# Performance work log

Measured on AMD Instinct MI355X. Metric: run time of the kernel, lower is better.

The kernel has to match this reference:

```python
import jax, jax.numpy as jnp
import numpy as np

EMBED_DIM = 512
NUM_HEADS = 8
TGT_LEN = 1024
BSZ = 16


def setup_inputs() -> dict:
    key = jax.random.key(0)
    ks = jax.random.split(key, 6)
    E = EMBED_DIM
    query = jax.random.normal(ks[0], (TGT_LEN, BSZ, E), jnp.float32)
    i_proj = jax.random.normal(ks[1], (3 * E,), jnp.float32)
    # xavier_uniform-ish scale for (3E, E)
    lim = (6.0 / (3 * E + E)) ** 0.5
    in_proj_weight = jax.random.uniform(ks[2], (3 * E, E), jnp.float32, -lim, lim)
    in_proj_bias = jnp.zeros((3 * E,), jnp.float32)
    lim2 = (6.0 / (2 * E)) ** 0.5
    out_w = jax.random.uniform(ks[3], (E, E), jnp.float32, -lim2, lim2)
    out_b = jnp.zeros((E,), jnp.float32)
    bias_k = jax.random.normal(ks[4], (1, 1, E), jnp.float32)
    bias_v = jax.random.normal(ks[5], (1, 1, E), jnp.float32)
    return dict(query=query, i_proj=i_proj, in_proj_weight=in_proj_weight,
                in_proj_bias=in_proj_bias, out_w=out_w, out_b=out_b,
                bias_k=bias_k, bias_v=bias_v)


def reference(query, i_proj, in_proj_weight, in_proj_bias, out_w, out_b, bias_k, bias_v):
    # qkv_same path: key = value = query (self-attention)
    T, B, E = query.shape
    H = NUM_HEADS
    hd = E // H
    scaling = hd ** -0.5
    # per-call weight mutation: every 3rd column replaced by i_proj
    w = in_proj_weight.at[:, ::3].set(i_proj[:, None])
    qkv = jnp.einsum('tbe,fe->tbf', query, w) + in_proj_bias  # (T, B, 3E)
    q, k, v = jnp.split(qkv, 3, axis=-1)
    q = q * scaling
    k = jnp.concatenate([k, jnp.broadcast_to(bias_k, (1, B, E))], axis=0)  # (T+1, B, E)
    v = jnp.concatenate([v, jnp.broadcast_to(bias_v, (1, B, E))], axis=0)
    S = k.shape[0]
    q = q.reshape(T, B * H, hd).transpose(1, 0, 2)  # (B*H, T, hd)
    k = k.reshape(S, B * H, hd).transpose(1, 0, 2)  # (B*H, S, hd)
    v = v.reshape(S, B * H, hd).transpose(1, 0, 2)
    aw = jnp.einsum('nth,nsh->nts', q, k)  # (B*H, T, S)
    # global min-max normalization over the entire score tensor (not softmax)
    mn = jnp.min(aw)
    mx = jnp.max(aw)
    aw = (aw - mn) / (mx - mn)
    attn = jnp.einsum('nts,nsh->nth', aw, v)  # (B*H, T, hd)
    attn = attn.transpose(1, 0, 2).reshape(T, B, E)
    attn = attn @ out_w.T + out_b  # out_proj
    aw_avg = aw.reshape(B, H, T, S).sum(axis=1) / H  # (B, T, S)
    wq, wk, wv = jnp.split(w, 3, axis=0)
    w_ret = jnp.stack([wq.T, wk.T, wv.T], axis=0)  # (3, E, E)
    return attn, aw_avg, w_ret
```

## Files before the change

kernel.cpp:

```cpp
#include <hip/hip_runtime.h>
#include <hip/hip_bf16.h>
#include <stdint.h>

typedef __bf16 bf16;
typedef __bf16 bf16x8 __attribute__((ext_vector_type(8)));
typedef __bf16 bf16x4 __attribute__((ext_vector_type(4)));
typedef float  f32x4  __attribute__((ext_vector_type(4)));

#define MFMA_BF16(a,b,c) __builtin_amdgcn_mfma_f32_16x16x32_bf16((a),(b),(c),0,0,0)

#define WS_QBF_IN  0L
#define WS_WBF     16777216L
#define WS_OUTWBF  18350080L
#define WS_Q       18874368L
#define WS_K       35651584L
#define WS_V       52428800L
#define WS_VT      69206016L
#define WS_AWLAST  85983232L
#define WS_VCS     86507520L
#define WS_MM      86540288L
#define WS_KT      86540544L
#define WS_KTV     103317760L

__device__ __forceinline__ void gload16(const void* g, void* l) {
  __builtin_amdgcn_global_load_lds((const __attribute__((address_space(1))) uint32_t*)g,
                                   (__attribute__((address_space(3))) uint32_t*)l, 16, 0, 0);
}
__device__ __forceinline__ unsigned ordf(float x) {
  unsigned b = __float_as_uint(x);
  return (b & 0x80000000u) ? ~b : (b | 0x80000000u);
}
__device__ __forceinline__ float deordf(unsigned u) {
  unsigned b = (u & 0x80000000u) ? (u ^ 0x80000000u) : ~u;
  return __uint_as_float(b);
}

__global__ __launch_bounds__(256) void cvt_query_kernel(const float* __restrict__ in,
                                                        bf16* __restrict__ out) {
  long i = (long)blockIdx.x * 256 + threadIdx.x;
  for (; i < 2097152L; i += (long)gridDim.x * 256) {
    float4 v = ((const float4*)in)[i];
    bf16x4 o; o[0] = (bf16)v.x; o[1] = (bf16)v.y; o[2] = (bf16)v.z; o[3] = (bf16)v.w;
    ((bf16x4*)out)[i] = o;
  }
}

__global__ __launch_bounds__(256) void prep_weights_kernel(
    const float* __restrict__ in_w, const float* __restrict__ i_proj,
    const float* __restrict__ out_w, bf16* __restrict__ w_bf,
    bf16* __restrict__ outw_bf, float* __restrict__ w_ret,
    unsigned* __restrict__ mm) {
  long idx = (long)blockIdx.x * 256 + threadIdx.x;
  if (idx == 0) { mm[0] = 0xFFFFFFFFu; mm[1] = 0u; }
  if (idx < 786432L) {
    int f = (int)(idx >> 9), e = (int)(idx & 511);
    float val = (e % 3 == 0) ? i_proj[f] : in_w[idx];
    w_bf[idx] = (bf16)val;
    w_ret[(long)(f >> 9) * 262144 + (long)e * 512 + (f & 511)] = val;
  } else if (idx < 1048576L) {
    long j = idx - 786432L;
    outw_bf[j] = (bf16)out_w[j];
  }
}

template <int MODE>
__global__ __launch_bounds__(256, 2) void gemm_kernel(
    const bf16* __restrict__ A, const bf16* __restrict__ B,
    const float* __restrict__ bias,
    bf16* __restrict__ q_out, bf16* __restrict__ k_out, bf16* __restrict__ v_out,
    float* __restrict__ outC) {
  const int K = 512;
  __shared__ __align__(16) bf16 aTile[128 * 32];
  __shared__ __align__(16) bf16 bTile[128 * 32];
  const int tid = threadIdx.x;
  const int lane = tid & 63, w = tid >> 6;
  const int l15 = lane & 15, l4 = lane >> 4;
  const long r0 = (long)blockIdx.y * 128;
  const long f0 = (long)blockIdx.x * 128;
  const int rm = (w >> 1) * 64, cn = (w & 1) * 64;
  const int srow = tid >> 2;
  const int scc = tid & 3;
  f32x4 acc[4][4] = {};

  for (int kk = 0; kk < K; kk += 32) {
#pragma unroll
    for (int i = 0; i < 2; ++i) {
      int row = srow + i * 64;
      int cc = scc ^ (row & 3);
      gload16(A + (r0 + row) * K + kk + cc * 8, (char*)aTile + (w * 64 + i * 256) * 16);
    }
#pragma unroll
    for (int i = 0; i < 2; ++i) {
      int row = srow + i * 64;
      int cc = scc ^ (row & 3);
      gload16(B + (f0 + row) * K + kk + cc * 8, (char*)bTile + (w * 64 + i * 256) * 16);
    }
    __syncthreads();
    bf16x8 af[4], bfr[4];
#pragma unroll
    for (int mi = 0; mi < 4; ++mi) {
      int r = rm + mi * 16 + l15;
      int c = l4 ^ (r & 3);
      af[mi] = *(const bf16x8*)((const char*)aTile + r * 64 + c * 16);
    }
#pragma unroll
    for (int ni = 0; ni < 4; ++ni) {
      int r = cn + ni * 16 + l15;
      int c = l4 ^ (r & 3);
      bfr[ni] = *(const bf16x8*)((const char*)bTile + r * 64 + c * 16);
    }
#pragma unroll
    for (int mi = 0; mi < 4; ++mi)
#pragma unroll
      for (int ni = 0; ni < 4; ++ni)
        acc[mi][ni] = MFMA_BF16(af[mi], bfr[ni], acc[mi][ni]);
    __syncthreads();
  }
#pragma unroll
  for (int mi = 0; mi < 4; ++mi)
#pragma unroll
    for (int ni = 0; ni < 4; ++ni)
#pragma unroll
      for (int r = 0; r < 4; ++r) {
        long row = r0 + rm + mi * 16 + l4 * 4 + r;
        int f = (int)f0 + cn + ni * 16 + l15;
        float val = acc[mi][ni][r] + bias[f];
        if (MODE == 0) {
          int t = (int)(row >> 4), b = (int)(row & 15);
          int which = f >> 9, hh = (f >> 6) & 7, d = f & 63;
          long off = ((long)(b * 8 + hh) * 1024 + t) * 64 + d;
          if (which == 0)      q_out[off] = (bf16)(val * 0.125f);
          else if (which == 1) k_out[off] = (bf16)val;
          else                 v_out[off] = (bf16)val;
        } else {
          outC[row * 512 + f] = val;
        }
      }
}

__global__ __launch_bounds__(256, 2) void awsum_gemm_kernel(
    const bf16* __restrict__ q_bf, const bf16* __restrict__ k_bf,
    const unsigned* __restrict__ mm, float* __restrict__ aw_out) {
  __shared__ __align__(16) bf16 aTile[128 * 32];
  __shared__ __align__(16) bf16 bTile[128 * 32];
  const int tid = threadIdx.x;
  const int lane = tid & 63, w = tid >> 6;
  const int l15 = lane & 15, l4 = lane >> 4;
  const int b = blockIdx.z;
  const int t0 = blockIdx.y * 128;
  const int s0 = blockIdx.x * 128;
  const int rm = (w >> 1) * 64, cn = (w & 1) * 64;
  const int srow = tid >> 2;
  const int scc = tid & 3;
  f32x4 acc[4][4] = {};

  for (int kk = 0; kk < 512; kk += 32) {
    int h = kk >> 6, db = kk & 63;
#pragma unroll
    for (int i = 0; i < 2; ++i) {
      int row = srow + i * 64;
      int cc = scc ^ (row & 3);
      gload16(q_bf + ((long)(b * 8 + h) * 1024 + t0 + row) * 64 + db + cc * 8,
              (char*)aTile + (w * 64 + i * 256) * 16);
    }
#pragma unroll
    for (int i = 0; i < 2; ++i) {
      int row = srow + i * 64;
      int cc = scc ^ (row & 3);
      gload16(k_bf + ((long)(b * 8 + h) * 1024 + s0 + row) * 64 + db + cc * 8,
              (char*)bTile + (w * 64 + i * 256) * 16);
    }
    __syncthreads();
    bf16x8 af[4], bfr[4];
#pragma unroll
    for (int mi = 0; mi < 4; ++mi) {
      int r = rm + mi * 16 + l15;
      int c = l4 ^ (r & 3);
      af[mi] = *(const bf16x8*)((const char*)aTile + r * 64 + c * 16);
    }
#pragma unroll
    for (int ni = 0; ni < 4; ++ni) {
      int r = cn + ni * 16 + l15;
      int c = l4 ^ (r & 3);
      bfr[ni] = *(const bf16x8*)((const char*)bTile + r * 64 + c * 16);
    }
#pragma unroll
    for (int mi = 0; mi < 4; ++mi)
#pragma unroll
      for (int ni = 0; ni < 4; ++ni)
        acc[mi][ni] = MFMA_BF16(af[mi], bfr[ni], acc[mi][ni]);
    __syncthreads();
  }
  float mn = deordf(mm[0]), mx = deordf(mm[1]);
  float a8 = 0.125f / (mx - mn), c = -mn * 8.f * a8;
#pragma unroll
  for (int mi = 0; mi < 4; ++mi)
#pragma unroll
    for (int ni = 0; ni < 4; ++ni)
#pragma unroll
      for (int r = 0; r < 4; ++r) {
        int t = t0 + rm + mi * 16 + l4 * 4 + r;
        int s = s0 + cn + ni * 16 + l15;
        aw_out[((long)b * 1024 + t) * 1025 + s] = fmaf(a8, acc[mi][ni][r], c);
      }
}

__global__ __launch_bounds__(256) void transpose_kv_kernel(
    const bf16* __restrict__ k_bf, const bf16* __restrict__ v_bf,
    bf16* __restrict__ kT, bf16* __restrict__ vT) {
  const bf16* src = blockIdx.z ? v_bf : k_bf;
  bf16* dst = blockIdx.z ? vT : kT;
  const int n = blockIdx.y;
  const long s0 = (long)blockIdx.x * 64;
  __shared__ __align__(16) bf16 tile[64][72];
  const int tid = threadIdx.x;
  const int row = tid >> 3, cc = tid & 7;
#pragma unroll
  for (int it = 0; it < 2; ++it) {
    int r = row + it * 32;
    bf16x8 vv = *(const bf16x8*)(src + ((long)n * 1024 + s0 + r) * 64 + cc * 8);
    *(bf16x8*)&tile[r][cc * 8] = vv;
  }
  __syncthreads();
#pragma unroll
  for (int it = 0; it < 2; ++it) {
    int d = row + it * 32;
    bf16x8 ov;
#pragma unroll
    for (int j = 0; j < 8; ++j) ov[j] = tile[cc * 8 + j][d];
    *(bf16x8*)(dst + ((long)n * 64 + d) * 1024 + s0 + cc * 8) = ov;
  }
}

__global__ __launch_bounds__(256) void vcolsum_kernel(const bf16* __restrict__ v_bf,
                                                      const float* __restrict__ bias_v,
                                                      float* __restrict__ vcs) {
  const int n = blockIdx.x, h = n & 7;
  const int d = threadIdx.x & 63, g = threadIdx.x >> 6;
  float acc = 0.f;
  const bf16* base = v_bf + (long)n * 65536 + d;
  for (int s = g * 256; s < g * 256 + 256; ++s) acc += (float)base[(long)s * 64];
  __shared__ float red[4][64];
  red[g][d] = acc;
  __syncthreads();
  if (g == 0) vcs[n * 64 + d] = red[0][d] + red[1][d] + red[2][d] + red[3][d] + bias_v[h * 64 + d];
}

__global__ __launch_bounds__(256, 2) void qkt_minmax_kernel(
    const bf16* __restrict__ q_bf, const bf16* __restrict__ k_bf,
    unsigned* __restrict__ mm) {
  const int tid = threadIdx.x;
  const int lane = tid & 63, w = tid >> 6;
  const int l15 = lane & 15, l4 = lane >> 4;
  const int d_ = blockIdx.x;
  const int xcd = d_ & 7, slot = d_ >> 3;
  const int b = xcd * 2 + (slot >> 6);
  const int rest = slot & 63;
  const int t0 = (rest >> 2) * 64;
  const int h = ((rest >> 1) & 1) * 4 + w;
  const int sh = rest & 1;
  const long n = (long)b * 8 + h;

  bf16x8 qf[4][2];
  const bf16* qbase = q_bf + (n * 1024 + t0) * 64;
#pragma unroll
  for (int mi = 0; mi < 4; ++mi)
#pragma unroll
    for (int ks = 0; ks < 2; ++ks)
      qf[mi][ks] = *(const bf16x8*)(qbase + (mi * 16 + l15) * 64 + ks * 32 + l4 * 8);

  const bf16* kbase = k_bf + n * 65536 + (long)sh * 32768;

  float vmin = 1e30f, vmax = -1e30f;
  for (int st = 0; st < 16; ++st) {
    const int s0 = st * 32;
    bf16x8 kf[4];
#pragma unroll
    for (int ks = 0; ks < 2; ++ks)
#pragma unroll
      for (int ni = 0; ni < 2; ++ni)
        kf[ks * 2 + ni] =
            *(const bf16x8*)(kbase + (long)(s0 + ni * 16 + l15) * 64 + ks * 32 + l4 * 8);
    f32x4 aw[4][2] = {};
#pragma unroll
    for (int ks = 0; ks < 2; ++ks)
#pragma unroll
      for (int mi = 0; mi < 4; ++mi)
#pragma unroll
        for (int ni = 0; ni < 2; ++ni)
          aw[mi][ni] = MFMA_BF16(qf[mi][ks], kf[ks * 2 + ni], aw[mi][ni]);
#pragma unroll
    for (int mi = 0; mi < 4; ++mi)
#pragma unroll
      for (int ni = 0; ni < 2; ++ni)
#pragma unroll
        for (int r = 0; r < 4; ++r) {
          vmin = fminf(vmin, aw[mi][ni][r]);
          vmax = fmaxf(vmax, aw[mi][ni][r]);
        }
  }
#pragma unroll
  for (int off = 32; off; off >>= 1) {
    vmin = fminf(vmin, __shfl_xor(vmin, off));
    vmax = fmaxf(vmax, __shfl_xor(vmax, off));
  }
  if (lane == 0) { atomicMin(&mm[0], ordf(vmin)); atomicMax(&mm[1], ordf(vmax)); }
}

__global__ __launch_bounds__(256) void ktv_kernel(const bf16* __restrict__ kT,
                                                  const bf16* __restrict__ vT,
                                                  bf16* __restrict__ ktvT) {
  const int n = blockIdx.x;
  const int tid = threadIdx.x;
  const int lane = tid & 63, w = tid >> 6;
  const int l15 = lane & 15, l4 = lane >> 4;
  const int wr = w >> 1, wc = w & 1;
  f32x4 acc[2][2] = {};
  const bf16* kbase = kT + (long)n * 65536;
  const bf16* vbase = vT + (long)n * 65536;
  for (int s0 = 0; s0 < 1024; s0 += 32) {
    bf16x8 af[2], bfr[2];
#pragma unroll
    for (int mi = 0; mi < 2; ++mi)
      af[mi] = *(const bf16x8*)(kbase + (long)(wr * 32 + mi * 16 + l15) * 1024 + s0 + l4 * 8);
#pragma unroll
    for (int ni = 0; ni < 2; ++ni)
      bfr[ni] = *(const bf16x8*)(vbase + (long)(wc * 32 + ni * 16 + l15) * 1024 + s0 + l4 * 8);
#pragma unroll
    for (int mi = 0; mi < 2; ++mi)
#pragma unroll
      for (int ni = 0; ni < 2; ++ni)
        acc[mi][ni] = MFMA_BF16(af[mi], bfr[ni], acc[mi][ni]);
  }
#pragma unroll
  for (int mi = 0; mi < 2; ++mi)
#pragma unroll
    for (int ni = 0; ni < 2; ++ni)
#pragma unroll
      for (int r = 0; r < 4; ++r) {
        int d = wr * 32 + mi * 16 + l4 * 4 + r;
        int dp = wc * 32 + ni * 16 + l15;
        ktvT[(long)n * 4096 + dp * 64 + d] = (bf16)acc[mi][ni][r];
      }
}

__global__ __launch_bounds__(256) void qattn_kernel(
    const bf16* __restrict__ q_bf, const bf16* __restrict__ ktvT,
    const float* __restrict__ aw_last, const float* __restrict__ vcs,
    const float* __restrict__ bias_v, const unsigned* __restrict__ mm,
    bf16* __restrict__ A2) {
  const int tid = threadIdx.x;
  const int lane = tid & 63, w = tid >> 6;
  const int l15 = lane & 15, l4 = lane >> 4;
  const int t0 = blockIdx.x * 64;
  const int h = blockIdx.y * 4 + w;
  const int b = blockIdx.z;
  const long n = (long)b * 8 + h;
  f32x4 acc[4][4] = {};
  const bf16* qbase = q_bf + (n * 1024 + t0) * 64;
  const bf16* kbase = ktvT + (long)n * 4096;
#pragma unroll
  for (int kk = 0; kk < 64; kk += 32) {
    bf16x8 af[4], bfr[4];
#pragma unroll
    for (int mi = 0; mi < 4; ++mi)
      af[mi] = *(const bf16x8*)(qbase + (mi * 16 + l15) * 64 + kk + l4 * 8);
#pragma unroll
    for (int ni = 0; ni < 4; ++ni)
      bfr[ni] = *(const bf16x8*)(kbase + (ni * 16 + l15) * 64 + kk + l4 * 8);
#pragma unroll
    for (int mi = 0; mi < 4; ++mi)
#pragma unroll
      for (int ni = 0; ni < 4; ++ni)
        acc[mi][ni] = MFMA_BF16(af[mi], bfr[ni], acc[mi][ni]);
  }
  float mn = deordf(mm[0]), mx = deordf(mm[1]);
  float a = 1.f / (mx - mn), c = -mn * a;
#pragma unroll
  for (int mi = 0; mi < 4; ++mi)
#pragma unroll
    for (int r = 0; r < 4; ++r) {
      int t = t0 + mi * 16 + l4 * 4 + r;
      float alast = a * aw_last[n * 1024 + t];
#pragma unroll
      for (int ni = 0; ni < 4; ++ni) {
        int dp = ni * 16 + l15;
        float val = a * acc[mi][ni][r] + alast * bias_v[h * 64 + dp] + c * vcs[n * 64 + dp];
        A2[((long)t * 16 + b) * 512 + h * 64 + dp] = (bf16)val;
      }
    }
}

__global__ __launch_bounds__(256) void bias_col_kernel(const bf16* __restrict__ q_bf,
                                                       const float* __restrict__ bias_k,
                                                       float* __restrict__ aw_last,
                                                       unsigned* __restrict__ mm) {
  const int n = blockIdx.y, h = n & 7;
  const int t = blockIdx.x * 256 + threadIdx.x;
  float acc = 0.f;
  const bf16* qrow = q_bf + ((long)n * 1024 + t) * 64;
#pragma unroll
  for (int j = 0; j < 8; ++j) {
    bf16x8 qv = *(const bf16x8*)(qrow + j * 8);
#pragma unroll
    for (int e = 0; e < 8; ++e) acc += (float)qv[e] * bias_k[h * 64 + j * 8 + e];
  }
  aw_last[(long)n * 1024 + t] = acc;
  float vmin = acc, vmax = acc;
#pragma unroll
  for (int off = 32; off; off >>= 1) {
    vmin = fminf(vmin, __shfl_xor(vmin, off));
    vmax = fmaxf(vmax, __shfl_xor(vmax, off));
  }
  if ((threadIdx.x & 63) == 0) { atomicMin(&mm[0], ordf(vmin)); atomicMax(&mm[1], ordf(vmax)); }
}

__global__ __launch_bounds__(256) void lastcol_kernel(const float* __restrict__ aw_last,
                                                      const unsigned* __restrict__ mm,
                                                      float* __restrict__ aw_out) {
  int idx = blockIdx.x * 256 + threadIdx.x;
  int b = idx >> 10, t = idx & 1023;
  float mn = deordf(mm[0]), mx = deordf(mm[1]);
  float a8 = 0.125f / (mx - mn), c = -mn * 8.f * a8;
  float sum = 0.f;
#pragma unroll
  for (int h = 0; h < 8; ++h) sum += aw_last[(long)(b * 8 + h) * 1024 + t];
  aw_out[((long)b * 1024 + t) * 1025 + 1024] = fmaf(a8, sum, c);
}

extern "C" void kernel_launch(void* const* d_in, const int* in_sizes, int n_in,
                              void* d_out, int out_size, void* d_ws, size_t ws_size,
                              hipStream_t stream) {
  const float* query  = (const float*)d_in[0];
  const float* i_proj = (const float*)d_in[1];
  const float* in_w   = (const float*)d_in[2];
  const float* in_b   = (const float*)d_in[3];
  const float* out_w  = (const float*)d_in[4];
  const float* out_b  = (const float*)d_in[5];
  const float* bias_k = (const float*)d_in[6];
  const float* bias_v = (const float*)d_in[7];
  float* out = (float*)d_out;

  char* ws = (char*)d_ws;
  bf16* qbf_in = (bf16*)(ws + WS_QBF_IN);
  bf16* w_bf   = (bf16*)(ws + WS_WBF);
  bf16* outwbf = (bf16*)(ws + WS_OUTWBF);
  bf16* q_bf   = (bf16*)(ws + WS_Q);
  bf16* k_bf   = (bf16*)(ws + WS_K);
  bf16* v_bf   = (bf16*)(ws + WS_V);
  bf16* vT     = (bf16*)(ws + WS_VT);
  bf16* kT     = (bf16*)(ws + WS_KT);
  bf16* ktvT   = (bf16*)(ws + WS_KTV);
  float* aw_last = (float*)(ws + WS_AWLAST);
  float* vcs     = (float*)(ws + WS_VCS);
  unsigned* mm   = (unsigned*)(ws + WS_MM);
  bf16* A2 = qbf_in;

  float* out_attn  = out;
  float* out_awavg = out + 8388608L;
  float* out_wret  = out + 25182208L;

  cvt_query_kernel<<<2048, 256, 0, stream>>>(query, qbf_in);
  prep_weights_kernel<<<4096, 256, 0, stream>>>(in_w, i_proj, out_w, w_bf, outwbf, out_wret, mm);
  gemm_kernel<0><<<dim3(12, 128), 256, 0, stream>>>(qbf_in, w_bf, in_b, q_bf, k_bf, v_bf, nullptr);
  transpose_kv_kernel<<<dim3(16, 128, 2), 256, 0, stream>>>(k_bf, v_bf, kT, vT);
  vcolsum_kernel<<<128, 256, 0, stream>>>(v_bf, bias_v, vcs);
  qkt_minmax_kernel<<<1024, 256, 0, stream>>>(q_bf, k_bf, mm);
  bias_col_kernel<<<dim3(4, 128), 256, 0, stream>>>(q_bf, bias_k, aw_last, mm);
  ktv_kernel<<<128, 256, 0, stream>>>(kT, vT, ktvT);
  awsum_gemm_kernel<<<dim3(8, 8, 16), 256, 0, stream>>>(q_bf, k_bf, mm, out_awavg);
  lastcol_kernel<<<64, 256, 0, stream>>>(aw_last, mm, out_awavg);
  qattn_kernel<<<dim3(16, 2, 16), 256, 0, stream>>>(q_bf, ktvT, aw_last, vcs, bias_v, mm, A2);
  gemm_kernel<1><<<dim3(4, 128), 256, 0, stream>>>(A2, outwbf, out_b, nullptr, nullptr, nullptr, out_attn);
}
```

Measured before the change: 337.0 us.

## Fuse global min-max into head-summed score GEMM and rescale in separate pass

Removes the standalone QK^T min/max kernel. The head-summed score GEMM now accumulates each head separately, folding per-head min/max into atomics and writing raw head sums. A new elementwise pass then normalises the whole (B,T,S+1) output, including the bias column. This avoids recomputing all QK^T products a second time, at the cost of an extra full read and write of the 67 MB averaged-weights output and more register pressure for the per-head accumulators.

Result: faster. 322.5 us (-4.3%).

```diff
diff --git a/kernel.cpp b/kernel.cpp
--- a/kernel.cpp
+++ b/kernel.cpp
@@ -140,7 +140,7 @@
 
 __global__ __launch_bounds__(256, 2) void awsum_gemm_kernel(
     const bf16* __restrict__ q_bf, const bf16* __restrict__ k_bf,
-    const unsigned* __restrict__ mm, float* __restrict__ aw_out) {
+    float* __restrict__ aw_raw, unsigned* __restrict__ mm) {
   __shared__ __align__(16) bf16 aTile[128 * 32];
   __shared__ __align__(16) bf16 bTile[128 * 32];
   const int tid = threadIdx.x;
@@ -153,6 +153,8 @@
   const int srow = tid >> 2;
   const int scc = tid & 3;
   f32x4 acc[4][4] = {};
+  f32x4 hsum[4][4] = {};
+  float vmin = 1e30f, vmax = -1e30f;
 
   for (int kk = 0; kk < 512; kk += 32) {
     int h = kk >> 6, db = kk & 63;
@@ -190,9 +192,21 @@
       for (int ni = 0; ni < 4; ++ni)
         acc[mi][ni] = MFMA_BF16(af[mi], bfr[ni], acc[mi][ni]);
     __syncthreads();
-  }
-  float mn = deordf(mm[0]), mx = deordf(mm[1]);
-  float a8 = 0.125f / (mx - mn), c = -mn * 8.f * a8;
+    if (kk & 32) {
+#pragma unroll
+      for (int mi = 0; mi < 4; ++mi)
+#pragma unroll
+        for (int ni = 0; ni < 4; ++ni) {
+#pragma unroll
+          for (int r = 0; r < 4; ++r) {
+            float v = acc[mi][ni][r];
+            vmin = fminf(vmin, v); vmax = fmaxf(vmax, v);
+            hsum[mi][ni][r] += v;
+          }
+          acc[mi][ni] = (f32x4){0.f, 0.f, 0.f, 0.f};
+        }
+    }
+  }
 #pragma unroll
   for (int mi = 0; mi < 4; ++mi)
 #pragma unroll
@@ -201,8 +215,14 @@
       for (int r = 0; r < 4; ++r) {
         int t = t0 + rm + mi * 16 + l4 * 4 + r;
         int s = s0 + cn + ni * 16 + l15;
-        aw_out[((long)b * 1024 + t) * 1025 + s] = fmaf(a8, acc[mi][ni][r], c);
+        aw_raw[((long)b * 1024 + t) * 1025 + s] = hsum[mi][ni][r];
       }
+#pragma unroll
+  for (int off = 32; off; off >>= 1) {
+    vmin = fminf(vmin, __shfl_xor(vmin, off));
+    vmax = fmaxf(vmax, __shfl_xor(vmax, off));
+  }
+  if (lane == 0) { atomicMin(&mm[0], ordf(vmin)); atomicMax(&mm[1], ordf(vmax)); }
 }
 
 __global__ __launch_bounds__(256) void transpose_kv_kernel(
@@ -244,67 +264,6 @@
   red[g][d] = acc;
   __syncthreads();
   if (g == 0) vcs[n * 64 + d] = red[0][d] + red[1][d] + red[2][d] + red[3][d] + bias_v[h * 64 + d];
-}
-
-__global__ __launch_bounds__(256, 2) void qkt_minmax_kernel(
-    const bf16* __restrict__ q_bf, const bf16* __restrict__ k_bf,
-    unsigned* __restrict__ mm) {
-  const int tid = threadIdx.x;
-  const int lane = tid & 63, w = tid >> 6;
-  const int l15 = lane & 15, l4 = lane >> 4;
-  const int d_ = blockIdx.x;
-  const int xcd = d_ & 7, slot = d_ >> 3;
-  const int b = xcd * 2 + (slot >> 6);
-  const int rest = slot & 63;
-  const int t0 = (rest >> 2) * 64;
-  const int h = ((rest >> 1) & 1) * 4 + w;
-  const int sh = rest & 1;
-  const long n = (long)b * 8 + h;
-
-  bf16x8 qf[4][2];
-  const bf16* qbase = q_bf + (n * 1024 + t0) * 64;
-#pragma unroll
-  for (int mi = 0; mi < 4; ++mi)
-#pragma unroll
-    for (int ks = 0; ks < 2; ++ks)
-      qf[mi][ks] = *(const bf16x8*)(qbase + (mi * 16 + l15) * 64 + ks * 32 + l4 * 8);
-
-  const bf16* kbase = k_bf + n * 65536 + (long)sh * 32768;
-
-  float vmin = 1e30f, vmax = -1e30f;
-  for (int st = 0; st < 16; ++st) {
-    const int s0 = st * 32;
-    bf16x8 kf[4];
-#pragma unroll
-    for (int ks = 0; ks < 2; ++ks)
-#pragma unroll
-      for (int ni = 0; ni < 2; ++ni)
-        kf[ks * 2 + ni] =
-            *(const bf16x8*)(kbase + (long)(s0 + ni * 16 + l15) * 64 + ks * 32 + l4 * 8);
-    f32x4 aw[4][2] = {};
-#pragma unroll
-    for (int ks = 0; ks < 2; ++ks)
-#pragma unroll
-      for (int mi = 0; mi < 4; ++mi)
-#pragma unroll
-        for (int ni = 0; ni < 2; ++ni)
-          aw[mi][ni] = MFMA_BF16(qf[mi][ks], kf[ks * 2 + ni], aw[mi][ni]);
-#pragma unroll
-    for (int mi = 0; mi < 4; ++mi)
-#pragma unroll
-      for (int ni = 0; ni < 2; ++ni)
-#pragma unroll
-        for (int r = 0; r < 4; ++r) {
-          vmin = fminf(vmin, aw[mi][ni][r]);
-          vmax = fmaxf(vmax, aw[mi][ni][r]);
-        }
-  }
-#pragma unroll
-  for (int off = 32; off; off >>= 1) {
-    vmin = fminf(vmin, __shfl_xor(vmin, off));
-    vmax = fmaxf(vmax, __shfl_xor(vmax, off));
-  }
-  if (lane == 0) { atomicMin(&mm[0], ordf(vmin)); atomicMax(&mm[1], ordf(vmax)); }
 }
 
 __global__ __launch_bounds__(256) void ktv_kernel(const bf16* __restrict__ kT,
@@ -415,17 +374,24 @@
   if ((threadIdx.x & 63) == 0) { atomicMin(&mm[0], ordf(vmin)); atomicMax(&mm[1], ordf(vmax)); }
 }
 
-__global__ __launch_bounds__(256) void lastcol_kernel(const float* __restrict__ aw_last,
-                                                      const unsigned* __restrict__ mm,
-                                                      float* __restrict__ aw_out) {
-  int idx = blockIdx.x * 256 + threadIdx.x;
-  int b = idx >> 10, t = idx & 1023;
+__global__ __launch_bounds__(256) void rescale_kernel(float* __restrict__ aw_out,
+                                                      const float* __restrict__ aw_last,
+                                                      const unsigned* __restrict__ mm) {
+  long idx = (long)blockIdx.x * 256 + threadIdx.x;
   float mn = deordf(mm[0]), mx = deordf(mm[1]);
-  float a8 = 0.125f / (mx - mn), c = -mn * 8.f * a8;
-  float sum = 0.f;
-#pragma unroll
-  for (int h = 0; h < 8; ++h) sum += aw_last[(long)(b * 8 + h) * 1024 + t];
-  aw_out[((long)b * 1024 + t) * 1025 + 1024] = fmaf(a8, sum, c);
+  float a = 1.f / (mx - mn), c = -mn * a;
+  int s = (int)(idx % 1025);
+  long bt = idx / 1025;
+  float v;
+  if (s < 1024) {
+    v = aw_out[idx];
+  } else {
+    int b = (int)(bt >> 10), t = (int)(bt & 1023);
+    v = 0.f;
+#pragma unroll
+    for (int h = 0; h < 8; ++h) v += aw_last[(long)(b * 8 + h) * 1024 + t];
+  }
+  aw_out[idx] = fmaf(a, v * 0.125f, c);
 }
 
 extern "C" void kernel_launch(void* const* d_in, const int* in_sizes, int n_in,
@@ -465,11 +431,10 @@
   gemm_kernel<0><<<dim3(12, 128), 256, 0, stream>>>(qbf_in, w_bf, in_b, q_bf, k_bf, v_bf, nullptr);
   transpose_kv_kernel<<<dim3(16, 128, 2), 256, 0, stream>>>(k_bf, v_bf, kT, vT);
   vcolsum_kernel<<<128, 256, 0, stream>>>(v_bf, bias_v, vcs);
-  qkt_minmax_kernel<<<1024, 256, 0, stream>>>(q_bf, k_bf, mm);
   bias_col_kernel<<<dim3(4, 128), 256, 0, stream>>>(q_bf, bias_k, aw_last, mm);
+  awsum_gemm_kernel<<<dim3(8, 8, 16), 256, 0, stream>>>(q_bf, k_bf, out_awavg, mm);
   ktv_kernel<<<128, 256, 0, stream>>>(kT, vT, ktvT);
-  awsum_gemm_kernel<<<dim3(8, 8, 16), 256, 0, stream>>>(q_bf, k_bf, mm, out_awavg);
-  lastcol_kernel<<<64, 256, 0, stream>>>(aw_last, mm, out_awavg);
+  rescale_kernel<<<65600, 256, 0, stream>>>(out_awavg, aw_last, mm);
   qattn_kernel<<<dim3(16, 2, 16), 256, 0, stream>>>(q_bf, ktvT, aw_last, vcs, bias_v, mm, A2);
   gemm_kernel<1><<<dim3(4, 128), 256, 0, stream>>>(A2, outwbf, out_b, nullptr, nullptr, nullptr, out_attn);
 }
```
